# Performance work log

Hardware: AMD Instinct MI355X
Metric: run time of the kernel (lower is better)

Reference implementation:

```python
import jax, jax.numpy as jnp
import numpy as np

IMG_SIZE = 1024.0  # image width == height in pixels
N_PTS = 2_000_000


def setup_inputs() -> dict:
    key = jax.random.key(0)
    k1, k2, k3 = jax.random.split(key, 3)
    # 2D screen-space gaussian centers, pixel coords in [0, IMG_SIZE)
    pos2d = jax.random.uniform(k1, (N_PTS, 2), dtype=jnp.float32) * IMG_SIZE
    # PSD 2x2 covariances: A A^T + 0.5 I (screen-space extent of a few pixels)
    A = 0.8 * jax.random.normal(k2, (N_PTS, 2, 2), dtype=jnp.float32)
    cov2d = jnp.einsum('nij,nkj->nik', A, A) + 0.5 * jnp.eye(2, dtype=jnp.float32)
    opacity = jax.random.uniform(k3, (N_PTS,), dtype=jnp.float32)
    return {"pos2d": pos2d, "cov2d": cov2d, "opacity": opacity, "num_tile": 16}


def reference(pos2d, cov2d, opacity, num_tile):
    # --- per-gaussian rasterization setup (radius + conic) ---
    a = cov2d[:, 0, 0]; b = cov2d[:, 0, 1]
    c = cov2d[:, 1, 0]; d = cov2d[:, 1, 1]
    trace = a + d
    det = a * d - b * c
    term1 = 0.5 * trace
    term2 = 0.5 * jnp.sqrt(jnp.clip(trace * trace - 4.0 * det, 0.0))
    # max eigenvalue of the 2x2 covariance, as in GaussianRender.get_radius
    radius = jnp.maximum(term1 - term2, term1 + term2)
    inv_det = 1.0 / det
    conic = jnp.stack([d * inv_det, -b * inv_det, a * inv_det], axis=-1)  # [N,3]

    # --- tile binning (histogram) ---
    tile_size = IMG_SIZE / num_tile
    tile_xy = jnp.clip(jnp.floor(pos2d / tile_size).astype(jnp.int32), 0, num_tile - 1)
    tile_id = tile_xy[:, 1] * num_tile + tile_xy[:, 0]  # [N] in [0, num_tile^2)
    n_tiles = num_tile * num_tile
    tile_counts = jax.ops.segment_sum(
        jnp.ones_like(tile_id), tile_id, num_segments=n_tiles)  # [T^2]
    cum = jnp.cumsum(tile_counts)
    tile_offsets = jnp.concatenate([jnp.zeros((1,), cum.dtype), cum[:-1]])  # exclusive

    # --- counting sort: stable argsort by tile id reorders gaussians per tile ---
    order = jnp.argsort(tile_id)  # stable
    feat = jnp.concatenate(
        [pos2d, conic, opacity[:, None], radius[:, None]], axis=1)  # [N,7]
    sorted_feat = feat[order]
    return sorted_feat, tile_counts, tile_offsets, order.astype(jnp.int32)
```

## Files before the change

### kernel.cpp

```cpp
#include <hip/hip_runtime.h>

#define NT 16
#define NTILES 256
#define INV_TILE (1.0f/64.0f)
#define CHUNK 2048

__device__ __forceinline__ int tile_of(float x, float y) {
    int tx = (int)floorf(x * INV_TILE);
    tx = tx < 0 ? 0 : (tx > NT - 1 ? NT - 1 : tx);
    int ty = (int)floorf(y * INV_TILE);
    ty = ty < 0 ? 0 : (ty > NT - 1 ? NT - 1 : ty);
    return ty * NT + tx;
}

__device__ __forceinline__ unsigned long long match_mask(int t, bool valid) {
    unsigned long long m = ~0ull;
#pragma unroll
    for (int b = 0; b < 8; ++b) {
        unsigned long long bal = __ballot((t >> b) & 1);
        m &= ((t >> b) & 1) ? bal : ~bal;
    }
    m &= __ballot(valid);
    return m;
}

__global__ __launch_bounds__(512) void k_hist(const float2* __restrict__ pos2d,
                                              int* __restrict__ gHist,
                                              int* __restrict__ gcounts,
                                              unsigned int* __restrict__ P,
                                              int N) {
    __shared__ int cnt[8][NTILES];
    __shared__ unsigned short pwr[CHUNK];
    __shared__ unsigned char  tld[CHUNK];
    __shared__ int wsum[4];
    const int tid = threadIdx.x;
    const int wl = tid >> 6, lane = tid & 63;
    const int base_i = blockIdx.x * CHUNK;
#pragma unroll
    for (int k = 0; k < 4; ++k) cnt[wl][lane + 64 * k] = 0;

#pragma unroll
    for (int r = 0; r < 4; ++r) {
        int o = wl * 256 + r * 64 + lane;
        int i = base_i + o;
        bool valid = i < N;
        int t = 0;
        if (valid) { float2 p = pos2d[i]; t = tile_of(p.x, p.y); }
        tld[o] = (unsigned char)t;
        unsigned long long m = match_mask(t, valid);
        if (valid) {
            unsigned long long below = m & ((1ull << lane) - 1ull);
            int rank = __popcll(below);
            int b = cnt[wl][t];
            if (below == 0ull) cnt[wl][t] = b + __popcll(m);
            pwr[o] = (unsigned short)(b + rank);
        }
    }
    __syncthreads();

    int c[8], tot = 0, x = 0;
    if (tid < NTILES) {
#pragma unroll
        for (int w = 0; w < 8; ++w) { c[w] = cnt[w][tid]; tot += c[w]; }
        gHist[(size_t)blockIdx.x * NTILES + tid] = tot;
        if (tot) atomicAdd(&gcounts[tid], tot);
        x = tot;
#pragma unroll
        for (int s = 1; s < 64; s <<= 1) {
            int y = __shfl_up(x, s);
            if (lane >= s) x += y;
        }
        if (lane == 63) wsum[wl] = x;
    }
    __syncthreads();
    if (tid < NTILES) {
        int wpre = 0;
        for (int u = 0; u < wl; ++u) wpre += wsum[u];
        int run = wpre + x - tot;
#pragma unroll
        for (int w = 0; w < 8; ++w) { cnt[w][tid] = run; run += c[w]; }
    }
    __syncthreads();

    int nvalid = N - base_i; if (nvalid > CHUNK) nvalid = CHUNK;
    for (int o = tid; o < nvalid; o += 512) {
        int t = tld[o];
        int ldest = cnt[o >> 8][t] + pwr[o];
        P[base_i + o] = ((unsigned int)t << 16) | (unsigned int)ldest;
    }
}

__global__ __launch_bounds__(256) void k_scan(const int* __restrict__ gcounts,
                                              int* __restrict__ gHist,
                                              float* __restrict__ out_counts,
                                              float* __restrict__ out_offsets,
                                              int NWA) {
    const int t = blockIdx.x;
    const int tid = threadIdx.x;
    const int wl = tid >> 6, lane = tid & 63;
    __shared__ int sdata[NTILES];
    __shared__ int wsum[4];

    int v = (tid < t) ? gcounts[tid] : 0;
    sdata[tid] = v;
    __syncthreads();
#pragma unroll
    for (int s = 128; s > 0; s >>= 1) {
        if (tid < s) sdata[tid] += sdata[tid + s];
        __syncthreads();
    }
    int offset_t = sdata[0];
    if (tid == 0) {
        int ct = gcounts[t];
        out_counts[t]  = (float)ct;
        out_offsets[t] = (float)offset_t;
        gHist[(size_t)NWA * NTILES + t] = offset_t + ct;
    }

    int vals[4];
    const int base_row = tid * 4;
#pragma unroll
    for (int k = 0; k < 4; ++k) {
        int row = base_row + k;
        vals[k] = (row < NWA) ? gHist[(size_t)row * NTILES + t] : 0;
    }
    int tv = vals[0] + vals[1] + vals[2] + vals[3];
    int x = tv;
#pragma unroll
    for (int s = 1; s < 64; s <<= 1) {
        int y = __shfl_up(x, s);
        if (lane >= s) x += y;
    }
    if (lane == 63) wsum[wl] = x;
    __syncthreads();
    int wprefix = 0;
    for (int u = 0; u < wl; ++u) wprefix += wsum[u];
    int running = offset_t + wprefix + (x - tv);
#pragma unroll
    for (int k = 0; k < 4; ++k) {
        int row = base_row + k;
        if (row < NWA) gHist[(size_t)row * NTILES + t] = running;
        running += vals[k];
    }
}

__global__ __launch_bounds__(512) void k_scatter(const float2* __restrict__ pos2d,
                                                 const float4* __restrict__ cov2d,
                                                 const float*  __restrict__ opacity,
                                                 const int*    __restrict__ gBase,
                                                 const unsigned int* __restrict__ P,
                                                 float* __restrict__ out_feat,
                                                 float* __restrict__ out_order,
                                                 int N) {
    __shared__ float fA[CHUNK], fB[CHUNK], fD[CHUNK];
    __shared__ unsigned int slotPk[CHUNK];
    __shared__ int gbase[NTILES];
    __shared__ int tstart[NTILES];
    __shared__ int wsum[4];

    const int tid = threadIdx.x;
    const int wl = tid >> 6, lane = tid & 63;
    const int base_i = blockIdx.x * CHUNK;

    int gb = 0, tot = 0, x = 0;
    if (tid < NTILES) {
        gb = gBase[(size_t)blockIdx.x * NTILES + tid];
        int ge = gBase[(size_t)(blockIdx.x + 1) * NTILES + tid];
        gbase[tid] = gb;
        tot = ge - gb;
        x = tot;
#pragma unroll
        for (int s = 1; s < 64; s <<= 1) {
            int y = __shfl_up(x, s);
            if (lane >= s) x += y;
        }
        if (lane == 63) wsum[wl] = x;
    }
    __syncthreads();
    if (tid < NTILES) {
        int wpre = 0;
        for (int u = 0; u < wl; ++u) wpre += wsum[u];
        tstart[tid] = wpre + x - tot;
    }
    __syncthreads();

    int nvalid = N - base_i; if (nvalid > CHUNK) nvalid = CHUNK;
    for (int o = tid; o < nvalid; o += 512) {
        int i = base_i + o;
        unsigned int pk = P[i];
        int t = pk >> 16;
        int ldest = pk & 0xFFFF;
        float4 cv = cov2d[i];
        fA[ldest] = cv.x; fB[ldest] = cv.y; fD[ldest] = cv.w;
        slotPk[ldest] = ((unsigned int)t << 16) | (unsigned int)o;
    }
    __syncthreads();

    for (int j = tid; j < nvalid; j += 512) {
        unsigned int pk = slotPk[j];
        int t = pk >> 16;
        int o = pk & 0xFFFF;
        int gdest = gbase[t] + (j - tstart[t]);
        int i = base_i + o;
        float2 p = pos2d[i];
        float op = opacity[i];
        float a = fA[j], b = fB[j], d = fD[j];
        float trace = a + d;
        float det = a * d - b * b;
        float term1 = 0.5f * trace;
        float term2 = 0.5f * sqrtf(fmaxf(trace * trace - 4.0f * det, 0.0f));
        float rad = fmaxf(term1 - term2, term1 + term2);
        float inv = 1.0f / det;
        float* fr = out_feat + (size_t)gdest * 7;
        fr[0] = p.x; fr[1] = p.y; fr[2] = d * inv; fr[3] = -b * inv;
        fr[4] = a * inv; fr[5] = op; fr[6] = rad;
        out_order[gdest] = (float)i;
    }
}

extern "C" void kernel_launch(void* const* d_in, const int* in_sizes, int n_in,
                              void* d_out, int out_size, void* d_ws, size_t ws_size,
                              hipStream_t stream) {
    const float2* pos2d   = (const float2*)d_in[0];
    const float4* cov2d   = (const float4*)d_in[1];
    const float*  opacity = (const float*)d_in[2];
    const int N = in_sizes[2];

    float* out         = (float*)d_out;
    float* out_feat    = out;
    float* out_counts  = out + (size_t)N * 7;
    float* out_offsets = out_counts + NTILES;
    float* out_order   = out_offsets + NTILES;

    int nchunks = (N + CHUNK - 1) / CHUNK;

    int* gcounts     = (int*)d_ws;
    int* gHist       = gcounts + NTILES;
    unsigned int* P  = (unsigned int*)(gHist + (size_t)(nchunks + 1) * NTILES);

    hipMemsetAsync(gcounts, 0, NTILES * sizeof(int), stream);
    k_hist<<<nchunks, 512, 0, stream>>>(pos2d, gHist, gcounts, P, N);
    k_scan<<<NTILES, 256, 0, stream>>>(gcounts, gHist, out_counts, out_offsets, nchunks);
    k_scatter<<<nchunks, 512, 0, stream>>>(pos2d, cov2d, opacity, gHist, P,
                                           out_feat, out_order, N);
}
```

Measured before the change: 159.2 us.

## Recompute per-chunk ranks in scatter and stage features in LDS for coalesced writes

Drops the intermediate P array: the histogram kernel now only counts, and the scatter kernel recomputes local tile ranks with wave ballots, so P is no longer written and re-read through global memory. Scatter now computes all seven features in a coalesced read pass, stores them in a padded shared-memory buffer, and writes the output as contiguous 7-float runs per tile segment instead of strided per-row stores. Chunk size is halved to 1024 with occupancy hints, which doubles the number of histogram rows the scan kernel must process (scan now runs 512 threads). The cost is duplicated ballot/rank work and more shared memory per block in scatter. The scan kernel's 4 rows per thread cover 2048 rows, which is enough for ~1954 chunks.

Measured after the change: 179.0 us. 12.4% more time.

```diff
diff --git a/kernel.cpp b/kernel.cpp
--- a/kernel.cpp
+++ b/kernel.cpp
@@ -3,7 +3,8 @@
 #define NT 16
 #define NTILES 256
 #define INV_TILE (1.0f/64.0f)
-#define CHUNK 2048
+#define CHUNK 1024
+#define FSTRIDE 1025
 
 __device__ __forceinline__ int tile_of(float x, float y) {
     int tx = (int)floorf(x * INV_TILE);
@@ -24,73 +25,42 @@
     return m;
 }
 
-__global__ __launch_bounds__(512) void k_hist(const float2* __restrict__ pos2d,
-                                              int* __restrict__ gHist,
-                                              int* __restrict__ gcounts,
-                                              unsigned int* __restrict__ P,
-                                              int N) {
-    __shared__ int cnt[8][NTILES];
-    __shared__ unsigned short pwr[CHUNK];
-    __shared__ unsigned char  tld[CHUNK];
-    __shared__ int wsum[4];
+__global__ __launch_bounds__(512, 8) void k_hist(const float2* __restrict__ pos2d,
+                                                 int* __restrict__ gHist,
+                                                 int* __restrict__ gcounts,
+                                                 int N) {
+    __shared__ unsigned short cnt[8][NTILES];
     const int tid = threadIdx.x;
     const int wl = tid >> 6, lane = tid & 63;
     const int base_i = blockIdx.x * CHUNK;
-#pragma unroll
-    for (int k = 0; k < 4; ++k) cnt[wl][lane + 64 * k] = 0;
-
-#pragma unroll
-    for (int r = 0; r < 4; ++r) {
-        int o = wl * 256 + r * 64 + lane;
+    ((int*)cnt)[tid] = 0;
+    ((int*)cnt)[tid + 512] = 0;
+    __syncthreads();
+#pragma unroll
+    for (int r = 0; r < 2; ++r) {
+        int o = wl * 128 + r * 64 + lane;
         int i = base_i + o;
         bool valid = i < N;
         int t = 0;
         if (valid) { float2 p = pos2d[i]; t = tile_of(p.x, p.y); }
-        tld[o] = (unsigned char)t;
         unsigned long long m = match_mask(t, valid);
         if (valid) {
             unsigned long long below = m & ((1ull << lane) - 1ull);
-            int rank = __popcll(below);
-            int b = cnt[wl][t];
-            if (below == 0ull) cnt[wl][t] = b + __popcll(m);
-            pwr[o] = (unsigned short)(b + rank);
-        }
-    }
-    __syncthreads();
-
-    int c[8], tot = 0, x = 0;
+            if (below == 0ull)
+                cnt[wl][t] = (unsigned short)(cnt[wl][t] + __popcll(m));
+        }
+    }
+    __syncthreads();
     if (tid < NTILES) {
-#pragma unroll
-        for (int w = 0; w < 8; ++w) { c[w] = cnt[w][tid]; tot += c[w]; }
+        int tot = 0;
+#pragma unroll
+        for (int w = 0; w < 8; ++w) tot += cnt[w][tid];
         gHist[(size_t)blockIdx.x * NTILES + tid] = tot;
         if (tot) atomicAdd(&gcounts[tid], tot);
-        x = tot;
-#pragma unroll
-        for (int s = 1; s < 64; s <<= 1) {
-            int y = __shfl_up(x, s);
-            if (lane >= s) x += y;
-        }
-        if (lane == 63) wsum[wl] = x;
-    }
-    __syncthreads();
-    if (tid < NTILES) {
-        int wpre = 0;
-        for (int u = 0; u < wl; ++u) wpre += wsum[u];
-        int run = wpre + x - tot;
-#pragma unroll
-        for (int w = 0; w < 8; ++w) { cnt[w][tid] = run; run += c[w]; }
-    }
-    __syncthreads();
-
-    int nvalid = N - base_i; if (nvalid > CHUNK) nvalid = CHUNK;
-    for (int o = tid; o < nvalid; o += 512) {
-        int t = tld[o];
-        int ldest = cnt[o >> 8][t] + pwr[o];
-        P[base_i + o] = ((unsigned int)t << 16) | (unsigned int)ldest;
-    }
-}
-
-__global__ __launch_bounds__(256) void k_scan(const int* __restrict__ gcounts,
+    }
+}
+
+__global__ __launch_bounds__(512) void k_scan(const int* __restrict__ gcounts,
                                               int* __restrict__ gHist,
                                               float* __restrict__ out_counts,
                                               float* __restrict__ out_offsets,
@@ -99,10 +69,9 @@
     const int tid = threadIdx.x;
     const int wl = tid >> 6, lane = tid & 63;
     __shared__ int sdata[NTILES];
-    __shared__ int wsum[4];
-
-    int v = (tid < t) ? gcounts[tid] : 0;
-    sdata[tid] = v;
+    __shared__ int wsum[8];
+
+    if (tid < NTILES) sdata[tid] = (tid < t) ? gcounts[tid] : 0;
     __syncthreads();
 #pragma unroll
     for (int s = 128; s > 0; s >>= 1) {
@@ -114,7 +83,6 @@
         int ct = gcounts[t];
         out_counts[t]  = (float)ct;
         out_offsets[t] = (float)offset_t;
-        gHist[(size_t)NWA * NTILES + t] = offset_t + ct;
     }
 
     int vals[4];
@@ -144,30 +112,74 @@
     }
 }
 
-__global__ __launch_bounds__(512) void k_scatter(const float2* __restrict__ pos2d,
-                                                 const float4* __restrict__ cov2d,
-                                                 const float*  __restrict__ opacity,
-                                                 const int*    __restrict__ gBase,
-                                                 const unsigned int* __restrict__ P,
-                                                 float* __restrict__ out_feat,
-                                                 float* __restrict__ out_order,
-                                                 int N) {
-    __shared__ float fA[CHUNK], fB[CHUNK], fD[CHUNK];
+__global__ __launch_bounds__(512, 8) void k_scatter(const float2* __restrict__ pos2d,
+                                                    const float4* __restrict__ cov2d,
+                                                    const float*  __restrict__ opacity,
+                                                    const int*    __restrict__ gBase,
+                                                    float* __restrict__ out_feat,
+                                                    float* __restrict__ out_order,
+                                                    int N) {
+    __shared__ float sFeat[7 * FSTRIDE];
     __shared__ unsigned int slotPk[CHUNK];
-    __shared__ int gbase[NTILES];
-    __shared__ int tstart[NTILES];
+    __shared__ unsigned short cnt[8][NTILES];
+    __shared__ int base7[NTILES];
+    __shared__ int obase[NTILES];
     __shared__ int wsum[4];
 
     const int tid = threadIdx.x;
     const int wl = tid >> 6, lane = tid & 63;
     const int base_i = blockIdx.x * CHUNK;
 
-    int gb = 0, tot = 0, x = 0;
+    ((int*)cnt)[tid] = 0;
+    ((int*)cnt)[tid + 512] = 0;
+    int gb = 0;
+    if (tid < NTILES) gb = gBase[(size_t)blockIdx.x * NTILES + tid];
+    __syncthreads();
+
+    unsigned int meta[2];
+#pragma unroll
+    for (int r = 0; r < 2; ++r) {
+        int o = wl * 128 + r * 64 + lane;
+        int i = base_i + o;
+        bool valid = i < N;
+        int t = 0;
+        if (valid) {
+            float2 p  = pos2d[i];
+            float4 cv = cov2d[i];
+            float op  = opacity[i];
+            t = tile_of(p.x, p.y);
+            float a = cv.x, b = cv.y, d = cv.w;
+            float trace = a + d;
+            float det = a * d - b * b;
+            float term1 = 0.5f * trace;
+            float term2 = 0.5f * sqrtf(fmaxf(trace * trace - 4.0f * det, 0.0f));
+            float rad = fmaxf(term1 - term2, term1 + term2);
+            float inv = 1.0f / det;
+            sFeat[0 * FSTRIDE + o] = p.x;
+            sFeat[1 * FSTRIDE + o] = p.y;
+            sFeat[2 * FSTRIDE + o] = d * inv;
+            sFeat[3 * FSTRIDE + o] = -b * inv;
+            sFeat[4 * FSTRIDE + o] = a * inv;
+            sFeat[5 * FSTRIDE + o] = op;
+            sFeat[6 * FSTRIDE + o] = rad;
+        }
+        unsigned long long m = match_mask(t, valid);
+        unsigned int pk = 0x80000000u;
+        if (valid) {
+            unsigned long long below = m & ((1ull << lane) - 1ull);
+            int rank = __popcll(below);
+            int b0 = cnt[wl][t];
+            if (below == 0ull) cnt[wl][t] = (unsigned short)(b0 + __popcll(m));
+            pk = ((unsigned)t << 16) | (unsigned)(b0 + rank);
+        }
+        meta[r] = pk;
+    }
+    __syncthreads();
+
+    int tot = 0, x = 0;
     if (tid < NTILES) {
-        gb = gBase[(size_t)blockIdx.x * NTILES + tid];
-        int ge = gBase[(size_t)(blockIdx.x + 1) * NTILES + tid];
-        gbase[tid] = gb;
-        tot = ge - gb;
+#pragma unroll
+        for (int w = 0; w < 8; ++w) tot += cnt[w][tid];
         x = tot;
 #pragma unroll
         for (int s = 1; s < 64; s <<= 1) {
@@ -180,41 +192,49 @@
     if (tid < NTILES) {
         int wpre = 0;
         for (int u = 0; u < wl; ++u) wpre += wsum[u];
-        tstart[tid] = wpre + x - tot;
+        int run = wpre + x - tot;
+        int ob = gb - run;
+        obase[tid] = ob;
+        base7[tid] = ob * 7;
+#pragma unroll
+        for (int w = 0; w < 8; ++w) {
+            int cw = cnt[w][tid];
+            cnt[w][tid] = (unsigned short)run;
+            run += cw;
+        }
+    }
+    __syncthreads();
+
+#pragma unroll
+    for (int r = 0; r < 2; ++r) {
+        unsigned int pk = meta[r];
+        if (!(pk & 0x80000000u)) {
+            int o = wl * 128 + r * 64 + lane;
+            int t  = pk >> 16;
+            int pw = pk & 0xFFFF;
+            int ldest = cnt[wl][t] + pw;
+            slotPk[ldest] = ((unsigned)t << 16) | (unsigned)o;
+        }
     }
     __syncthreads();
 
     int nvalid = N - base_i; if (nvalid > CHUNK) nvalid = CHUNK;
-    for (int o = tid; o < nvalid; o += 512) {
-        int i = base_i + o;
-        unsigned int pk = P[i];
-        int t = pk >> 16;
-        int ldest = pk & 0xFFFF;
-        float4 cv = cov2d[i];
-        fA[ldest] = cv.x; fB[ldest] = cv.y; fD[ldest] = cv.w;
-        slotPk[ldest] = ((unsigned int)t << 16) | (unsigned int)o;
-    }
-    __syncthreads();
-
+    int nv7 = nvalid * 7;
+    {
+        int j = (int)((unsigned)tid / 7u);
+        int c = tid - 7 * j;
+        for (int f = tid; f < nv7; f += 512) {
+            unsigned int pk = slotPk[j];
+            int t = pk >> 16;
+            int o = pk & 0xFFFF;
+            out_feat[(size_t)(base7[t] + f)] = sFeat[c * FSTRIDE + o];
+            j += 73; c += 1;
+            if (c >= 7) { c -= 7; j += 1; }
+        }
+    }
     for (int j = tid; j < nvalid; j += 512) {
         unsigned int pk = slotPk[j];
-        int t = pk >> 16;
-        int o = pk & 0xFFFF;
-        int gdest = gbase[t] + (j - tstart[t]);
-        int i = base_i + o;
-        float2 p = pos2d[i];
-        float op = opacity[i];
-        float a = fA[j], b = fB[j], d = fD[j];
-        float trace = a + d;
-        float det = a * d - b * b;
-        float term1 = 0.5f * trace;
-        float term2 = 0.5f * sqrtf(fmaxf(trace * trace - 4.0f * det, 0.0f));
-        float rad = fmaxf(term1 - term2, term1 + term2);
-        float inv = 1.0f / det;
-        float* fr = out_feat + (size_t)gdest * 7;
-        fr[0] = p.x; fr[1] = p.y; fr[2] = d * inv; fr[3] = -b * inv;
-        fr[4] = a * inv; fr[5] = op; fr[6] = rad;
-        out_order[gdest] = (float)i;
+        out_order[obase[pk >> 16] + j] = (float)(base_i + (int)(pk & 0xFFFF));
     }
 }
 
@@ -234,13 +254,12 @@
 
     int nchunks = (N + CHUNK - 1) / CHUNK;
 
-    int* gcounts     = (int*)d_ws;
-    int* gHist       = gcounts + NTILES;
-    unsigned int* P  = (unsigned int*)(gHist + (size_t)(nchunks + 1) * NTILES);
+    int* gcounts = (int*)d_ws;
+    int* gHist   = gcounts + NTILES;
 
     hipMemsetAsync(gcounts, 0, NTILES * sizeof(int), stream);
-    k_hist<<<nchunks, 512, 0, stream>>>(pos2d, gHist, gcounts, P, N);
-    k_scan<<<NTILES, 256, 0, stream>>>(gcounts, gHist, out_counts, out_offsets, nchunks);
-    k_scatter<<<nchunks, 512, 0, stream>>>(pos2d, cov2d, opacity, gHist, P,
+    k_hist<<<nchunks, 512, 0, stream>>>(pos2d, gHist, gcounts, N);
+    k_scan<<<NTILES, 512, 0, stream>>>(gcounts, gHist, out_counts, out_offsets, nchunks);
+    k_scatter<<<nchunks, 512, 0, stream>>>(pos2d, cov2d, opacity, gHist,
                                            out_feat, out_order, N);
 }
```
